# Kernel optimization log

Hardware: AMD Instinct MI355X
Metric: run time of the kernel (lower is better)

The kernel has to match this reference:

```python
import jax, jax.numpy as jnp
import numpy as np


def setup_inputs() -> dict:
    key = jax.random.key(0)
    k1, k2, k3 = jax.random.split(key, 3)
    B, N, C_IN, C_OUT = 8, 2048, 128, 64
    x = jax.random.normal(k1, (B, N, C_IN), dtype=jnp.float32)
    # Linear(c_in, c_out): weight [c_out, c_in], bias [c_out]
    W_adj = jax.random.normal(k2, (C_OUT, C_IN), dtype=jnp.float32) * (1.0 / np.sqrt(C_IN))
    b_adj = jax.random.normal(k3, (C_OUT,), dtype=jnp.float32) * 0.01
    return {"x": x, "W_adj": W_adj, "b_adj": b_adj}


def reference(x, W_adj, b_adj):
    # e_x = adj_projection(x): [B, N, C_out]
    e_x = jnp.einsum("bnc,oc->bno", x, W_adj) + b_adj
    # The original loop/concat builds all (i, j) pairs and takes per-pair
    # inner products; this is exactly the Gram matrix e_x @ e_x^T.
    lp = jax.nn.relu(jnp.tanh(jnp.einsum("bic,bjc->bij", e_x, e_x)))  # [B, N, N]
    num_neighbours = x.shape[1]
    node_feats = jnp.einsum("bij,bjc->bic", lp, e_x) / num_neighbours
    return node_feats, lp
```

## Files before the change

kernel.cpp:

```cpp
#include <hip/hip_runtime.h>
#include <hip/hip_bf16.h>


#define B_    8
#define N_    2048
#define D_    64
#define CIN_  128

typedef __bf16 bf16x8 __attribute__((ext_vector_type(8)));
typedef float f32x4  __attribute__((ext_vector_type(4)));

union FragU { uint4 u; bf16x8 f; };

static __device__ __forceinline__ bf16x8 ld_frag(const __hip_bfloat16* p) {
    FragU fu; fu.u = *reinterpret_cast<const uint4*>(p); return fu.f;
}

static __device__ __forceinline__ void split8(const float* p, bf16x8& hi, bf16x8& lo) {
    const float4 a = *reinterpret_cast<const float4*>(p);
    const float4 b = *reinterpret_cast<const float4*>(p + 4);
    const float v[8] = {a.x, a.y, a.z, a.w, b.x, b.y, b.z, b.w};
#pragma unroll
    for (int i = 0; i < 8; i++) {
        const __bf16 h = (__bf16)v[i];
        hi[i] = h;
        lo[i] = (__bf16)(v[i] - (float)h);
    }
}

static __device__ __forceinline__ bf16x8 cvt8(const float* p) {
    const float4 a = *reinterpret_cast<const float4*>(p);
    const float4 b = *reinterpret_cast<const float4*>(p + 4);
    bf16x8 r;
    r[0] = (__bf16)a.x; r[1] = (__bf16)a.y; r[2] = (__bf16)a.z; r[3] = (__bf16)a.w;
    r[4] = (__bf16)b.x; r[5] = (__bf16)b.y; r[6] = (__bf16)b.z; r[7] = (__bf16)b.w;
    return r;
}

__global__ __launch_bounds__(256) void ex_kernel(
    const float* __restrict__ x,
    const float* __restrict__ W,
    const float* __restrict__ bias,
    __hip_bfloat16* __restrict__ e_hi,
    __hip_bfloat16* __restrict__ e_lo,
    __hip_bfloat16* __restrict__ e_hiT)
{
    const int tid  = threadIdx.x;
    const int w    = tid >> 6;
    const int lane = tid & 63;
    const int quad = lane >> 4;
    const int l16  = lane & 15;
    const int m0   = blockIdx.x * 64 + w * 16;

    const float* xrow = x + (size_t)(m0 + l16) * CIN_;
    bf16x8 ah[4], al[4];
#pragma unroll
    for (int ks = 0; ks < 4; ks++)
        split8(xrow + ks * 32 + quad * 8, ah[ks], al[ks]);

    f32x4 acc[4];
#pragma unroll
    for (int nt = 0; nt < 4; nt++) acc[nt] = f32x4{0.f, 0.f, 0.f, 0.f};

#pragma unroll
    for (int ks = 0; ks < 4; ks++) {
#pragma unroll
        for (int nt = 0; nt < 4; nt++) {
            bf16x8 wh, wl;
            split8(W + (size_t)(nt * 16 + l16) * CIN_ + ks * 32 + quad * 8, wh, wl);
            acc[nt] = __builtin_amdgcn_mfma_f32_16x16x32_bf16(ah[ks], wh, acc[nt], 0, 0, 0);
            acc[nt] = __builtin_amdgcn_mfma_f32_16x16x32_bf16(ah[ks], wl, acc[nt], 0, 0, 0);
            acc[nt] = __builtin_amdgcn_mfma_f32_16x16x32_bf16(al[ks], wh, acc[nt], 0, 0, 0);
        }
    }

#pragma unroll
    for (int nt = 0; nt < 4; nt++) {
        const int chan = nt * 16 + l16;
        const float bv = bias[chan];
#pragma unroll
        for (int i = 0; i < 4; i++) {
            const int gr = m0 + quad * 4 + i;
            const float e = acc[nt][i] + bv;
            const __hip_bfloat16 hi = __float2bfloat16(e);
            const __hip_bfloat16 lo = __float2bfloat16(e - __bfloat162float(hi));
            e_hi[(size_t)gr * D_ + chan] = hi;
            e_lo[(size_t)gr * D_ + chan] = lo;
            const int bt = gr >> 11, ir = gr & (N_ - 1);
            e_hiT[((size_t)bt * D_ + chan) * N_ + ir] = hi;
        }
    }
}

#define LDE  72
#define LDT  136
#define LDF  132

__global__ __launch_bounds__(512) void fused_kernel(
    const __hip_bfloat16* __restrict__ e_hi,
    const __hip_bfloat16* __restrict__ e_lo,
    const __hip_bfloat16* __restrict__ e_hiT,
    float* __restrict__ out)
{
    __shared__ __align__(16) unsigned char smem[64 * LDF * 4 + 128 * LDE * 2 * 2 + 64 * LDT * 2];
    float*          sLpF  = (float*)smem;
    __hip_bfloat16* sEhi  = (__hip_bfloat16*)(smem + 64 * LDF * 4);
    __hip_bfloat16* sElo  = sEhi + 128 * LDE;
    __hip_bfloat16* sEhiT = sElo + 128 * LDE;

    const int b   = blockIdx.x;
    const int i0  = blockIdx.y * 64;
    const int tid = threadIdx.x;
    const int w = tid >> 6, lane = tid & 63, quad = lane >> 4, l16 = lane & 15;
    const int g = w >> 1, h = w & 1;
    const int m0 = i0 + g * 16;

    const __hip_bfloat16* eih = e_hi + (size_t)(b * N_ + m0 + l16) * D_;
    const __hip_bfloat16* eil = e_lo + (size_t)(b * N_ + m0 + l16) * D_;
    bf16x8 ahi[2], alo[2];
#pragma unroll
    for (int ks = 0; ks < 2; ks++) {
        ahi[ks] = ld_frag(eih + ks * 32 + quad * 8);
        alo[ks] = ld_frag(eil + ks * 32 + quad * 8);
    }

    f32x4 o[4];
#pragma unroll
    for (int nt = 0; nt < 4; nt++) o[nt] = f32x4{0.f, 0.f, 0.f, 0.f};

    float* lp_out = out + (size_t)B_ * N_ * D_;

    for (int jt = 0; jt < 16; jt++) {
        const int j0 = jt * 128;
        __syncthreads();

#pragma unroll
        for (int p = 0; p < 2; p++) {
            const int q = tid + p * 512;
            {
                const int r = q >> 3, c = (q & 7) * 8;
                *(uint4*)(sEhi + r * LDE + c) =
                    *(const uint4*)(e_hi + (size_t)(b * N_ + j0 + r) * D_ + c);
                *(uint4*)(sElo + r * LDE + c) =
                    *(const uint4*)(e_lo + (size_t)(b * N_ + j0 + r) * D_ + c);
            }
            {
                const int r = q >> 4, c = (q & 15) * 8;
                *(uint4*)(sEhiT + r * LDT + c) =
                    *(const uint4*)(e_hiT + (size_t)(b * D_ + r) * N_ + j0 + c);
            }
        }
        __syncthreads();

#pragma unroll
        for (int nt = 0; nt < 4; nt++) {
            const int n0 = h * 64 + nt * 16;
            f32x4 s = f32x4{0.f, 0.f, 0.f, 0.f};
#pragma unroll
            for (int ks = 0; ks < 2; ks++) {
                const int koff = ks * 32 + quad * 8;
                bf16x8 bhi = ld_frag(sEhi + (n0 + l16) * LDE + koff);
                bf16x8 blo = ld_frag(sElo + (n0 + l16) * LDE + koff);
                s = __builtin_amdgcn_mfma_f32_16x16x32_bf16(ahi[ks], bhi, s, 0, 0, 0);
                s = __builtin_amdgcn_mfma_f32_16x16x32_bf16(ahi[ks], blo, s, 0, 0, 0);
                s = __builtin_amdgcn_mfma_f32_16x16x32_bf16(alo[ks], bhi, s, 0, 0, 0);
            }
#pragma unroll
            for (int i = 0; i < 4; i++) {
                const float tc = fmaxf(s[i], 0.0f);
                const float z = __builtin_amdgcn_exp2f(tc * -2.8853900817779268f);
                const float v = (1.0f - z) * __builtin_amdgcn_rcpf(1.0f + z);
                const int row = g * 16 + quad * 4 + i;
                const int col = n0 + l16;
                sLpF[row * LDF + col] = v;
            }
        }
        __syncthreads();

#pragma unroll
        for (int ks = 0; ks < 2; ks++) {
            const int koff = h * 64 + ks * 32 + quad * 8;
            bf16x8 a = cvt8(sLpF + (g * 16 + l16) * LDF + koff);
#pragma unroll
            for (int nt = 0; nt < 4; nt++) {
                bf16x8 bfr = ld_frag(sEhiT + (nt * 16 + l16) * LDT + koff);
                o[nt] = __builtin_amdgcn_mfma_f32_16x16x32_bf16(a, bfr, o[nt], 0, 0, 0);
            }
        }

#pragma unroll
        for (int p = 0; p < 4; p++) {
            const int q = tid + p * 512;
            const int r = q >> 5, c = (q & 31) * 4;
            *(float4*)(lp_out + ((size_t)(b * N_ + i0 + r)) * N_ + j0 + c) =
                *(const float4*)(sLpF + r * LDF + c);
        }
    }

    __syncthreads();
    float* sO = (float*)smem;
#pragma unroll
    for (int nt = 0; nt < 4; nt++) {
#pragma unroll
        for (int i = 0; i < 4; i++) {
            const int row = quad * 4 + i;
            const int chan = nt * 16 + l16;
            sO[w * 1024 + row * 64 + chan] = o[nt][i];
        }
    }
    __syncthreads();
#pragma unroll
    for (int p = 0; p < 8; p++) {
        const int q = tid + p * 512;
        const int row = q >> 6, chan = q & 63;
        const int gg = row >> 4, rr = row & 15;
        const float v = sO[(2 * gg) * 1024 + rr * 64 + chan] +
                        sO[(2 * gg + 1) * 1024 + rr * 64 + chan];
        out[((size_t)(b * N_ + i0 + row)) * D_ + chan] = v * (1.0f / 2048.0f);
    }
}

extern "C" void kernel_launch(void* const* d_in, const int* in_sizes, int n_in,
                              void* d_out, int out_size, void* d_ws, size_t ws_size,
                              hipStream_t stream) {
    const float* x    = (const float*)d_in[0];
    const float* W    = (const float*)d_in[1];
    const float* bias = (const float*)d_in[2];
    float* out = (float*)d_out;

    __hip_bfloat16* e_hi  = (__hip_bfloat16*)d_ws;
    __hip_bfloat16* e_lo  = e_hi + (size_t)B_ * N_ * D_;
    __hip_bfloat16* e_hiT = e_lo + (size_t)B_ * N_ * D_;

    ex_kernel<<<dim3(256), dim3(256), 0, stream>>>(x, W, bias, e_hi, e_lo, e_hiT);
    fused_kernel<<<dim3(8, 32), dim3(512), 0, stream>>>(e_hi, e_lo, e_hiT, out);
}
```

Before: 180.3 us.

## Halve row tile, stage split weights in LDS, vectorize and nontemporal stores

The fused kernel now handles 32 query rows per block instead of 64, doubling the grid to 512 blocks. Each wave pair now covers a quarter of the column tile, and the final reduction sums four partial accumulators with float4 loads. The lp stores are moved before the second GEMM and use nontemporal stores, and launch bounds request 4 blocks per CU. In ex_kernel, W is split to bf16 hi/lo once into LDS, and the transposed e_hi stores are packed into 8-byte writes. The trade-off is that each block reloads the full E tiles for half as many rows, doubling total E traffic.

```diff
diff --git a/kernel.cpp b/kernel.cpp
--- a/kernel.cpp
+++ b/kernel.cpp
@@ -14,6 +14,10 @@
 
 static __device__ __forceinline__ bf16x8 ld_frag(const __hip_bfloat16* p) {
     FragU fu; fu.u = *reinterpret_cast<const uint4*>(p); return fu.f;
+}
+
+static __device__ __forceinline__ void st_frag(__hip_bfloat16* p, bf16x8 f) {
+    FragU fu; fu.f = f; *reinterpret_cast<uint4*>(p) = fu.u;
 }
 
 static __device__ __forceinline__ void split8(const float* p, bf16x8& hi, bf16x8& lo) {
@@ -36,6 +40,8 @@
     r[4] = (__bf16)b.x; r[5] = (__bf16)b.y; r[6] = (__bf16)b.z; r[7] = (__bf16)b.w;
     return r;
 }
+
+#define LDW  136
 
 __global__ __launch_bounds__(256) void ex_kernel(
     const float* __restrict__ x,
@@ -45,7 +51,23 @@
     __hip_bfloat16* __restrict__ e_lo,
     __hip_bfloat16* __restrict__ e_hiT)
 {
+    __shared__ __align__(16) __hip_bfloat16 sW[2 * 64 * LDW];
+    __hip_bfloat16* sWhi = sW;
+    __hip_bfloat16* sWlo = sW + 64 * LDW;
+
     const int tid  = threadIdx.x;
+
+#pragma unroll
+    for (int p = 0; p < 4; p++) {
+        const int q = tid + p * 256;
+        const int r = q >> 4, c = (q & 15) * 8;
+        bf16x8 hi, lo;
+        split8(W + (size_t)r * CIN_ + c, hi, lo);
+        st_frag(sWhi + r * LDW + c, hi);
+        st_frag(sWlo + r * LDW + c, lo);
+    }
+    __syncthreads();
+
     const int w    = tid >> 6;
     const int lane = tid & 63;
     const int quad = lane >> 4;
@@ -66,8 +88,8 @@
     for (int ks = 0; ks < 4; ks++) {
 #pragma unroll
         for (int nt = 0; nt < 4; nt++) {
-            bf16x8 wh, wl;
-            split8(W + (size_t)(nt * 16 + l16) * CIN_ + ks * 32 + quad * 8, wh, wl);
+            bf16x8 wh = ld_frag(sWhi + (nt * 16 + l16) * LDW + ks * 32 + quad * 8);
+            bf16x8 wl = ld_frag(sWlo + (nt * 16 + l16) * LDW + ks * 32 + quad * 8);
             acc[nt] = __builtin_amdgcn_mfma_f32_16x16x32_bf16(ah[ks], wh, acc[nt], 0, 0, 0);
             acc[nt] = __builtin_amdgcn_mfma_f32_16x16x32_bf16(ah[ks], wl, acc[nt], 0, 0, 0);
             acc[nt] = __builtin_amdgcn_mfma_f32_16x16x32_bf16(al[ks], wh, acc[nt], 0, 0, 0);
@@ -78,6 +100,7 @@
     for (int nt = 0; nt < 4; nt++) {
         const int chan = nt * 16 + l16;
         const float bv = bias[chan];
+        union { __hip_bfloat16 h[4]; uint2 u2; } hv;
 #pragma unroll
         for (int i = 0; i < 4; i++) {
             const int gr = m0 + quad * 4 + i;
@@ -86,9 +109,11 @@
             const __hip_bfloat16 lo = __float2bfloat16(e - __bfloat162float(hi));
             e_hi[(size_t)gr * D_ + chan] = hi;
             e_lo[(size_t)gr * D_ + chan] = lo;
-            const int bt = gr >> 11, ir = gr & (N_ - 1);
-            e_hiT[((size_t)bt * D_ + chan) * N_ + ir] = hi;
-        }
+            hv.h[i] = hi;
+        }
+        const int gr0 = m0 + quad * 4;
+        const int bt = gr0 >> 11, ir = gr0 & (N_ - 1);
+        *reinterpret_cast<uint2*>(e_hiT + ((size_t)bt * D_ + chan) * N_ + ir) = hv.u2;
     }
 }
 
@@ -96,23 +121,23 @@
 #define LDT  136
 #define LDF  132
 
-__global__ __launch_bounds__(512) void fused_kernel(
+__global__ __launch_bounds__(512, 4) void fused_kernel(
     const __hip_bfloat16* __restrict__ e_hi,
     const __hip_bfloat16* __restrict__ e_lo,
     const __hip_bfloat16* __restrict__ e_hiT,
     float* __restrict__ out)
 {
-    __shared__ __align__(16) unsigned char smem[64 * LDF * 4 + 128 * LDE * 2 * 2 + 64 * LDT * 2];
+    __shared__ __align__(16) unsigned char smem[32 * LDF * 4 + 128 * LDE * 2 * 2 + 64 * LDT * 2];
     float*          sLpF  = (float*)smem;
-    __hip_bfloat16* sEhi  = (__hip_bfloat16*)(smem + 64 * LDF * 4);
+    __hip_bfloat16* sEhi  = (__hip_bfloat16*)(smem + 32 * LDF * 4);
     __hip_bfloat16* sElo  = sEhi + 128 * LDE;
     __hip_bfloat16* sEhiT = sElo + 128 * LDE;
 
     const int b   = blockIdx.x;
-    const int i0  = blockIdx.y * 64;
+    const int i0  = blockIdx.y * 32;
     const int tid = threadIdx.x;
     const int w = tid >> 6, lane = tid & 63, quad = lane >> 4, l16 = lane & 15;
-    const int g = w >> 1, h = w & 1;
+    const int g = w >> 2, h = w & 3;
     const int m0 = i0 + g * 16;
 
     const __hip_bfloat16* eih = e_hi + (size_t)(b * N_ + m0 + l16) * D_;
@@ -153,8 +178,8 @@
         __syncthreads();
 
 #pragma unroll
-        for (int nt = 0; nt < 4; nt++) {
-            const int n0 = h * 64 + nt * 16;
+        for (int nt = 0; nt < 2; nt++) {
+            const int n0 = h * 32 + nt * 16;
             f32x4 s = f32x4{0.f, 0.f, 0.f, 0.f};
 #pragma unroll
             for (int ks = 0; ks < 2; ks++) {
@@ -178,8 +203,16 @@
         __syncthreads();
 
 #pragma unroll
-        for (int ks = 0; ks < 2; ks++) {
-            const int koff = h * 64 + ks * 32 + quad * 8;
+        for (int p = 0; p < 2; p++) {
+            const int q = tid + p * 512;
+            const int r = q >> 5, c = (q & 31) * 4;
+            __builtin_nontemporal_store(
+                *(const f32x4*)(sLpF + r * LDF + c),
+                (f32x4*)(lp_out + ((size_t)(b * N_ + i0 + r)) * N_ + j0 + c));
+        }
+
+        {
+            const int koff = h * 32 + quad * 8;
             bf16x8 a = cvt8(sLpF + (g * 16 + l16) * LDF + koff);
 #pragma unroll
             for (int nt = 0; nt < 4; nt++) {
@@ -187,14 +220,6 @@
                 o[nt] = __builtin_amdgcn_mfma_f32_16x16x32_bf16(a, bfr, o[nt], 0, 0, 0);
             }
         }
-
-#pragma unroll
-        for (int p = 0; p < 4; p++) {
-            const int q = tid + p * 512;
-            const int r = q >> 5, c = (q & 31) * 4;
-            *(float4*)(lp_out + ((size_t)(b * N_ + i0 + r)) * N_ + j0 + c) =
-                *(const float4*)(sLpF + r * LDF + c);
-        }
     }
 
     __syncthreads();
@@ -205,18 +230,26 @@
         for (int i = 0; i < 4; i++) {
             const int row = quad * 4 + i;
             const int chan = nt * 16 + l16;
-            sO[w * 1024 + row * 64 + chan] = o[nt][i];
+            sO[w * 1088 + row * 68 + chan] = o[nt][i];
         }
     }
     __syncthreads();
-#pragma unroll
-    for (int p = 0; p < 8; p++) {
-        const int q = tid + p * 512;
-        const int row = q >> 6, chan = q & 63;
+    {
+        const int row = tid >> 4;
+        const int c4  = (tid & 15) * 4;
         const int gg = row >> 4, rr = row & 15;
-        const float v = sO[(2 * gg) * 1024 + rr * 64 + chan] +
-                        sO[(2 * gg + 1) * 1024 + rr * 64 + chan];
-        out[((size_t)(b * N_ + i0 + row)) * D_ + chan] = v * (1.0f / 2048.0f);
+        const float* base = sO + (gg * 4) * 1088 + rr * 68 + c4;
+        const float4 v0 = *(const float4*)(base);
+        const float4 v1 = *(const float4*)(base + 1088);
+        const float4 v2 = *(const float4*)(base + 2176);
+        const float4 v3 = *(const float4*)(base + 3264);
+        f32x4 r;
+        r[0] = (v0.x + v1.x + v2.x + v3.x) * (1.0f / 2048.0f);
+        r[1] = (v0.y + v1.y + v2.y + v3.y) * (1.0f / 2048.0f);
+        r[2] = (v0.z + v1.z + v2.z + v3.z) * (1.0f / 2048.0f);
+        r[3] = (v0.w + v1.w + v2.w + v3.w) * (1.0f / 2048.0f);
+        __builtin_nontemporal_store(
+            r, (f32x4*)(out + ((size_t)(b * N_ + i0 + row)) * D_ + c4));
     }
 }
 
@@ -233,5 +266,5 @@
     __hip_bfloat16* e_hiT = e_lo + (size_t)B_ * N_ * D_;
 
     ex_kernel<<<dim3(256), dim3(256), 0, stream>>>(x, W, bias, e_hi, e_lo, e_hiT);
-    fused_kernel<<<dim3(8, 32), dim3(512), 0, stream>>>(e_hi, e_lo, e_hiT, out);
-}
+    fused_kernel<<<dim3(8, 64), dim3(512), 0, stream>>>(e_hi, e_lo, e_hiT, out);
+}
```

Result: faster. 175.1 us (-2.9%).
